# Kernel tuning notes

Measured on AMD Instinct MI355X. Metric: run time of the kernel, lower is better.

## Reference

```python
import jax, jax.numpy as jnp
import numpy as np


def make_grid(rows, cols):
    x = np.linspace(-1, 1, cols)
    y = np.linspace(-1, 1, rows)
    X, Y = np.meshgrid(x, y)
    pts = np.stack((X.flatten(), Y.flatten()), axis=-1)
    return jnp.asarray(pts, dtype=jnp.float32)


def setup_inputs() -> dict:
    key = jax.random.key(0)
    k1, k2, k3 = jax.random.split(key, 3)
    I, R, rows, cols = 32, 128, 128, 128
    centers = jax.random.normal(k1, (I, R, 2), dtype=jnp.float32)
    covariances = jax.random.uniform(k2, (I, R, 3), dtype=jnp.float32)
    amplitudes = jax.random.normal(k3, (I, R, 1), dtype=jnp.float32)
    grid = make_grid(rows, cols)  # (rows*cols, 2) in [-1, 1]
    return {"centers": centers, "covariances": covariances,
            "amplitudes": amplitudes, "grid": grid,
            "rows": rows, "cols": cols}


def reference(centers, covariances, amplitudes, grid, rows, cols):
    # centers: (I, R, 2); covariances: (I, R, 3) = [sxx, syy, sxy];
    # amplitudes: (I, R, 1); grid: (P, 2) with P = rows*cols.
    I = centers.shape[0]
    # diff components, (I, R, P) each -- avoids materializing (I, R, P, 2)
    dx = grid[:, 0][None, None, :] - centers[..., 0:1]
    dy = grid[:, 1][None, None, :] - centers[..., 1:2]
    a = covariances[..., 0:1]  # (I, R, 1)
    b = covariances[..., 1:2]
    c = covariances[..., 2:3]
    # quadratic form d^T M d with M = [[a, c], [c, b]]
    q = a * dx * dx + b * dy * dy + 2.0 * c * dx * dy  # (I, R, P)
    z = jnp.sum(jnp.exp(-0.5 * q) * amplitudes, axis=1)  # (I, P)
    z = z.reshape(I, 1, rows, cols)
    return jax.nn.sigmoid(z)
```

## Files before the change

### kernel.cpp

```cpp
#include <hip/hip_runtime.h>

#define NPIX 2
#define R_MAX 128

__global__ __launch_bounds__(256) void rbf_kernel(
    const float* __restrict__ centers,
    const float* __restrict__ covs,
    const float* __restrict__ amps,
    const float* __restrict__ grid,
    float* __restrict__ out,
    int R, int P, int blocksPerImage)
{
    __shared__ float4 s_c[R_MAX][2];

    const int img   = blockIdx.x / blocksPerImage;
    const int chunk = blockIdx.x % blocksPerImage;
    const int base  = chunk * (256 * NPIX);

    constexpr float S = -0.72134752044448170f;

    for (int r = threadIdx.x; r < R; r += 256) {
        const float2 cc = *(const float2*)(centers + (size_t)(img * R + r) * 2);
        const float* cv = covs + (size_t)(img * R + r) * 3;
        const float a = cv[0], b = cv[1], c = cv[2];
        const float amp = amps[img * R + r];
        const float sa = a * S;
        const float sb = b * S;
        const float sc = 2.0f * c * S;
        const float k1 = -2.0f * (a * cc.x + c * cc.y) * S;
        const float k2 = -2.0f * (b * cc.y + c * cc.x) * S;
        const float k0 = (a * cc.x * cc.x + b * cc.y * cc.y + 2.0f * c * cc.x * cc.y) * S;
        s_c[r][0] = make_float4(sa, sb, sc, k1);
        s_c[r][1] = make_float4(k2, k0, amp, 0.0f);
    }
    __syncthreads();

    float gx[NPIX], gy[NPIX], X[NPIX], Y[NPIX], XY[NPIX];
    float zA[NPIX], zB[NPIX];
    #pragma unroll
    for (int k = 0; k < NPIX; ++k) {
        const int p = base + k * 256 + (int)threadIdx.x;
        float2 g = make_float2(0.0f, 0.0f);
        if (p < P) g = *(const float2*)(grid + (size_t)p * 2);
        gx[k] = g.x; gy[k] = g.y;
        X[k]  = g.x * g.x;
        Y[k]  = g.y * g.y;
        XY[k] = g.x * g.y;
        zA[k] = 0.0f; zB[k] = 0.0f;
    }

    #pragma unroll 2
    for (int r = 0; r < R; r += 2) {
        const float4 a0 = s_c[r][0];
        const float4 a1 = s_c[r][1];
        const float4 b0 = s_c[r + 1][0];
        const float4 b1 = s_c[r + 1][1];
        #pragma unroll
        for (int k = 0; k < NPIX; ++k) {
            float t0 = fmaf(a0.x, X[k],
                       fmaf(a0.y, Y[k],
                       fmaf(a0.z, XY[k],
                       fmaf(a0.w, gx[k],
                       fmaf(a1.x, gy[k], a1.y)))));
            float t1 = fmaf(b0.x, X[k],
                       fmaf(b0.y, Y[k],
                       fmaf(b0.z, XY[k],
                       fmaf(b0.w, gx[k],
                       fmaf(b1.x, gy[k], b1.y)))));
            float e0, e1;
            asm("v_exp_f32 %0, %1" : "=v"(e0) : "v"(t0));
            asm("v_exp_f32 %0, %1" : "=v"(e1) : "v"(t1));
            zA[k] = fmaf(a1.z, e0, zA[k]);
            zB[k] = fmaf(b1.z, e1, zB[k]);
        }
    }

    #pragma unroll
    for (int k = 0; k < NPIX; ++k) {
        const int p = base + k * 256 + (int)threadIdx.x;
        if (p < P) {
            const float z = zA[k] + zB[k];
            const float ez = __expf(-z);
            out[(size_t)img * P + p] = 1.0f / (1.0f + ez);
        }
    }
}

extern "C" void kernel_launch(void* const* d_in, const int* in_sizes, int n_in,
                              void* d_out, int out_size, void* d_ws, size_t ws_size,
                              hipStream_t stream) {
    const float* centers = (const float*)d_in[0];
    const float* covs    = (const float*)d_in[1];
    const float* amps    = (const float*)d_in[2];
    const float* grid    = (const float*)d_in[3];
    float* out = (float*)d_out;

    const int P = in_sizes[3] / 2;
    const int I = out_size / P;
    const int R = in_sizes[2] / I;

    const int bpi = (P + 256 * NPIX - 1) / (256 * NPIX);
    rbf_kernel<<<I * bpi, 256, 0, stream>>>(centers, covs, amps, grid, out, R, P, bpi);
}
```

Measured before the change: 22.78 us.

## Precompute RBF coefficients in a prep kernel and read them from global memory

Moves the per-center coefficient computation into a separate prep kernel that writes 8 floats per center to workspace. The main kernel then reads those coefficients directly from global memory (uniform, so scalar or broadcast loads) instead of staging them in LDS behind a barrier. The sigmoid epilogue also switches to exp2 plus a reciprocal intrinsic. The price is an extra kernel launch and a global round trip for the coefficients. A fallback kernel keeps the old LDS path for when the workspace is too small.

```diff
diff --git a/kernel.cpp b/kernel.cpp
--- a/kernel.cpp
+++ b/kernel.cpp
@@ -1,39 +1,49 @@
 #include <hip/hip_runtime.h>
 
-#define NPIX 2
 #define R_MAX 128
 
-__global__ __launch_bounds__(256) void rbf_kernel(
+#if __has_builtin(__builtin_amdgcn_exp2f)
+__device__ __forceinline__ float fast_exp2(float x) { return __builtin_amdgcn_exp2f(x); }
+#else
+__device__ __forceinline__ float fast_exp2(float x) {
+    float e; asm("v_exp_f32 %0, %1" : "=v"(e) : "v"(x)); return e;
+}
+#endif
+
+__global__ __launch_bounds__(256) void rbf_prep(
     const float* __restrict__ centers,
     const float* __restrict__ covs,
     const float* __restrict__ amps,
+    float* __restrict__ coef,
+    int total)
+{
+    const int i = blockIdx.x * 256 + (int)threadIdx.x;
+    if (i >= total) return;
+    constexpr float S = -0.72134752044448170f;
+    const float cx = centers[2 * i], cy = centers[2 * i + 1];
+    const float a = covs[3 * i], b = covs[3 * i + 1], c = covs[3 * i + 2];
+    float* o = coef + (size_t)i * 8;
+    o[0] = a * S;
+    o[1] = b * S;
+    o[2] = 2.0f * c * S;
+    o[3] = -2.0f * (a * cx + c * cy) * S;
+    o[4] = -2.0f * (b * cy + c * cx) * S;
+    o[5] = (a * cx * cx + b * cy * cy + 2.0f * c * cx * cy) * S;
+    o[6] = amps[i];
+    o[7] = 0.0f;
+}
+
+#define NPIX 2
+__global__ __launch_bounds__(256) void rbf_main(
+    const float* __restrict__ coef,
     const float* __restrict__ grid,
     float* __restrict__ out,
     int R, int P, int blocksPerImage)
 {
-    __shared__ float4 s_c[R_MAX][2];
-
     const int img   = blockIdx.x / blocksPerImage;
     const int chunk = blockIdx.x % blocksPerImage;
     const int base  = chunk * (256 * NPIX);
-
-    constexpr float S = -0.72134752044448170f;
-
-    for (int r = threadIdx.x; r < R; r += 256) {
-        const float2 cc = *(const float2*)(centers + (size_t)(img * R + r) * 2);
-        const float* cv = covs + (size_t)(img * R + r) * 3;
-        const float a = cv[0], b = cv[1], c = cv[2];
-        const float amp = amps[img * R + r];
-        const float sa = a * S;
-        const float sb = b * S;
-        const float sc = 2.0f * c * S;
-        const float k1 = -2.0f * (a * cc.x + c * cc.y) * S;
-        const float k2 = -2.0f * (b * cc.y + c * cc.x) * S;
-        const float k0 = (a * cc.x * cc.x + b * cc.y * cc.y + 2.0f * c * cc.x * cc.y) * S;
-        s_c[r][0] = make_float4(sa, sb, sc, k1);
-        s_c[r][1] = make_float4(k2, k0, amp, 0.0f);
-    }
-    __syncthreads();
+    const float* __restrict__ cf = coef + (size_t)img * R * 8;
 
     float gx[NPIX], gy[NPIX], X[NPIX], Y[NPIX], XY[NPIX];
     float zA[NPIX], zB[NPIX];
@@ -51,10 +61,10 @@
 
     #pragma unroll 2
     for (int r = 0; r < R; r += 2) {
-        const float4 a0 = s_c[r][0];
-        const float4 a1 = s_c[r][1];
-        const float4 b0 = s_c[r + 1][0];
-        const float4 b1 = s_c[r + 1][1];
+        const float4 a0 = *(const float4*)(cf + 8 * r);
+        const float4 a1 = *(const float4*)(cf + 8 * r + 4);
+        const float4 b0 = *(const float4*)(cf + 8 * r + 8);
+        const float4 b1 = *(const float4*)(cf + 8 * r + 12);
         #pragma unroll
         for (int k = 0; k < NPIX; ++k) {
             float t0 = fmaf(a0.x, X[k],
@@ -67,21 +77,75 @@
                        fmaf(b0.z, XY[k],
                        fmaf(b0.w, gx[k],
                        fmaf(b1.x, gy[k], b1.y)))));
-            float e0, e1;
-            asm("v_exp_f32 %0, %1" : "=v"(e0) : "v"(t0));
-            asm("v_exp_f32 %0, %1" : "=v"(e1) : "v"(t1));
+            const float e0 = fast_exp2(t0);
+            const float e1 = fast_exp2(t1);
             zA[k] = fmaf(a1.z, e0, zA[k]);
             zB[k] = fmaf(b1.z, e1, zB[k]);
         }
     }
 
+    constexpr float L2E = 1.4426950408889634f;
     #pragma unroll
     for (int k = 0; k < NPIX; ++k) {
         const int p = base + k * 256 + (int)threadIdx.x;
         if (p < P) {
             const float z = zA[k] + zB[k];
-            const float ez = __expf(-z);
-            out[(size_t)img * P + p] = 1.0f / (1.0f + ez);
+            const float e = fast_exp2(-z * L2E);
+            out[(size_t)img * P + p] = __frcp_rn(1.0f + e);
+        }
+    }
+}
+
+__global__ __launch_bounds__(256) void rbf_fallback(
+    const float* __restrict__ centers, const float* __restrict__ covs,
+    const float* __restrict__ amps, const float* __restrict__ grid,
+    float* __restrict__ out, int R, int P, int blocksPerImage)
+{
+    __shared__ float4 s_c[R_MAX][2];
+    const int img   = blockIdx.x / blocksPerImage;
+    const int chunk = blockIdx.x % blocksPerImage;
+    const int base  = chunk * (256 * NPIX);
+    constexpr float S = -0.72134752044448170f;
+
+    for (int r = threadIdx.x; r < R; r += 256) {
+        const float2 cc = *(const float2*)(centers + (size_t)(img * R + r) * 2);
+        const float* cv = covs + (size_t)(img * R + r) * 3;
+        const float a = cv[0], b = cv[1], c = cv[2];
+        const float amp = amps[img * R + r];
+        s_c[r][0] = make_float4(a * S, b * S, 2.0f * c * S,
+                                -2.0f * (a * cc.x + c * cc.y) * S);
+        s_c[r][1] = make_float4(-2.0f * (b * cc.y + c * cc.x) * S,
+                                (a * cc.x * cc.x + b * cc.y * cc.y + 2.0f * c * cc.x * cc.y) * S,
+                                amp, 0.0f);
+    }
+    __syncthreads();
+
+    float gx[NPIX], gy[NPIX], X[NPIX], Y[NPIX], XY[NPIX], z[NPIX];
+    #pragma unroll
+    for (int k = 0; k < NPIX; ++k) {
+        const int p = base + k * 256 + (int)threadIdx.x;
+        float2 g = make_float2(0.0f, 0.0f);
+        if (p < P) g = *(const float2*)(grid + (size_t)p * 2);
+        gx[k] = g.x; gy[k] = g.y;
+        X[k] = g.x * g.x; Y[k] = g.y * g.y; XY[k] = g.x * g.y; z[k] = 0.0f;
+    }
+    for (int r = 0; r < R; ++r) {
+        const float4 c0 = s_c[r][0];
+        const float4 c1 = s_c[r][1];
+        #pragma unroll
+        for (int k = 0; k < NPIX; ++k) {
+            float t = fmaf(c0.x, X[k], fmaf(c0.y, Y[k], fmaf(c0.z, XY[k],
+                      fmaf(c0.w, gx[k], fmaf(c1.x, gy[k], c1.y)))));
+            z[k] = fmaf(c1.z, fast_exp2(t), z[k]);
+        }
+    }
+    constexpr float L2E = 1.4426950408889634f;
+    #pragma unroll
+    for (int k = 0; k < NPIX; ++k) {
+        const int p = base + k * 256 + (int)threadIdx.x;
+        if (p < P) {
+            const float e = fast_exp2(-z[k] * L2E);
+            out[(size_t)img * P + p] = __frcp_rn(1.0f + e);
         }
     }
 }
@@ -98,7 +162,15 @@
     const int P = in_sizes[3] / 2;
     const int I = out_size / P;
     const int R = in_sizes[2] / I;
+    const int total = I * R;
+    const int bpi = (P + 256 * NPIX - 1) / (256 * NPIX);
 
-    const int bpi = (P + 256 * NPIX - 1) / (256 * NPIX);
-    rbf_kernel<<<I * bpi, 256, 0, stream>>>(centers, covs, amps, grid, out, R, P, bpi);
+    const size_t need = (size_t)total * 8 * sizeof(float);
+    if (ws_size >= need) {
+        float* coef = (float*)d_ws;
+        rbf_prep<<<(total + 255) / 256, 256, 0, stream>>>(centers, covs, amps, coef, total);
+        rbf_main<<<I * bpi, 256, 0, stream>>>(coef, grid, out, R, P, bpi);
+    } else {
+        rbf_fallback<<<I * bpi, 256, 0, stream>>>(centers, covs, amps, grid, out, R, P, bpi);
+    }
 }
```

Result: slower. 32.65 us (+43.4%).
